# Kernel optimization log

Measured on AMD Instinct MI355X. Metric: run time of the kernel, lower is better.

## Reference

```python
import jax, jax.numpy as jnp
import numpy as np

B, L, P = 2, 1024, 1024
HID = 2048
NH, NKV, D = 32, 8, 64
T = P + L
N_REPEAT = NH // NKV
SCALE = D ** -0.5
NEG_INF = -1e9


def _rotate_half(x):
    x1, x2 = jnp.split(x, 2, axis=-1)
    return jnp.concatenate([-x2, x1], axis=-1)


def _apply_rope(q, k, cos, sin):
    # cos/sin: [L, D] -> broadcast to [1, 1, L, D]
    cos = cos[None, None, :, :]
    sin = sin[None, None, :, :]
    q = q * cos + _rotate_half(q) * sin
    k = k * cos + _rotate_half(k) * sin
    return q, k


def setup_inputs() -> dict:
    key = jax.random.key(0)
    ks = jax.random.split(key, 10)
    s = 0.02
    x = jax.random.normal(ks[0], (B, L, HID), jnp.float32)
    Wq = jax.random.normal(ks[1], (HID, NH * D), jnp.float32) * s
    bq = jnp.zeros((NH * D,), jnp.float32)
    Wk = jax.random.normal(ks[2], (HID, NKV * D), jnp.float32) * s
    bk = jnp.zeros((NKV * D,), jnp.float32)
    Wv = jax.random.normal(ks[3], (HID, NKV * D), jnp.float32) * s
    bv = jnp.zeros((NKV * D,), jnp.float32)
    Wo = jax.random.normal(ks[4], (NH * D, HID), jnp.float32) * s
    past_k = jax.random.normal(ks[5], (B, NKV, P, D), jnp.float32)
    past_v = jax.random.normal(ks[6], (B, NKV, P, D), jnp.float32)
    # RoPE tables for the L new positions (offsets P..P+L-1)
    pos = jnp.arange(P, P + L, dtype=jnp.float32)
    inv_freq = 1.0 / (10000.0 ** (jnp.arange(0, D, 2, dtype=jnp.float32) / D))
    freqs = pos[:, None] * inv_freq[None, :]            # [L, D/2]
    emb = jnp.concatenate([freqs, freqs], axis=-1)       # [L, D]
    cos = jnp.cos(emb)
    sin = jnp.sin(emb)
    # causal additive mask over total kv length T (past always visible)
    i = jnp.arange(L)[:, None]
    j = jnp.arange(T)[None, :]
    m = jnp.where(j <= i + P, 0.0, NEG_INF).astype(jnp.float32)  # [L, T]
    attention_mask = jnp.broadcast_to(m[None, None], (B, 1, L, T))
    return {
        "x": x, "attention_mask": attention_mask, "cos": cos, "sin": sin,
        "past_k": past_k, "past_v": past_v,
        "Wq": Wq, "bq": bq, "Wk": Wk, "bk": bk, "Wv": Wv, "bv": bv, "Wo": Wo,
    }


def reference(x, attention_mask, cos, sin, past_k, past_v, Wq, bq, Wk, bk, Wv, bv, Wo):
    # QKV projections
    q = (x @ Wq + bq).reshape(B, L, NH, D).transpose(0, 2, 1, 3)    # [B,NH,L,D]
    k = (x @ Wk + bk).reshape(B, L, NKV, D).transpose(0, 2, 1, 3)   # [B,NKV,L,D]
    v = (x @ Wv + bv).reshape(B, L, NKV, D).transpose(0, 2, 1, 3)
    q, k = _apply_rope(q, k, cos, sin)
    # KV-cache append
    k = jnp.concatenate([past_k, k], axis=2)  # [B,NKV,T,D]
    v = jnp.concatenate([past_v, v], axis=2)
    # repeat_kv for GQA
    if N_REPEAT > 1:
        k = jnp.repeat(k, N_REPEAT, axis=1)   # [B,NH,T,D]
        v = jnp.repeat(v, N_REPEAT, axis=1)
    w = jnp.einsum("bhld,bhtd->bhlt", q, k) * SCALE
    w = w + attention_mask
    w = jax.nn.softmax(w, axis=-1)
    out = jnp.einsum("bhlt,bhtd->bhld", w, v)
    out = out.transpose(0, 2, 1, 3).reshape(B, L, NH * D)
    return out @ Wo
```

## Files before the change

kernel.cpp:

```cpp
#include <hip/hip_runtime.h>
#include <stdint.h>

#define Bc   2
#define Lc   1024
#define Pc   1024
#define Tc   2048
#define HIDc 2048
#define NHc  32
#define NKVc 8
#define Dc   64

typedef __bf16 bf16x8 __attribute__((ext_vector_type(8)));
typedef float f32x4 __attribute__((ext_vector_type(4)));
typedef float f32x16 __attribute__((ext_vector_type(16)));

__device__ inline unsigned short f2bf(float f) {
  union { float f; uint32_t u; } v; v.f = f;
  uint32_t u = v.u;
  uint32_t r = (u + 0x7fffu + ((u >> 16) & 1u)) >> 16;
  return (unsigned short)r;
}
__device__ inline float bf2f(unsigned short h) {
  union { uint32_t u; float f; } v; v.u = ((uint32_t)h) << 16;
  return v.f;
}
__device__ inline float exp2_fast(float x) {
#if defined(__has_builtin)
#if __has_builtin(__builtin_amdgcn_exp2f)
  return __builtin_amdgcn_exp2f(x);
#else
  return exp2f(x);
#endif
#else
  return exp2f(x);
#endif
}
__device__ inline unsigned int cvtpk_bf16(float a, float b) {
  unsigned int r;
  asm("v_cvt_pk_bf16_f32 %0, %1, %2" : "=v"(r) : "v"(a), "v"(b));
  return r;
}
__device__ inline void plane32_swap(unsigned int& a, unsigned int& b) {
  asm("v_permlane32_swap_b32 %0, %1" : "+v"(a), "+v"(b));
}

typedef const __attribute__((address_space(1))) unsigned int* gas1_t;
typedef __attribute__((address_space(3))) unsigned int* las3_t;
__device__ inline void gload_lds16(const void* g, void* l) {
  __builtin_amdgcn_global_load_lds((gas1_t)g, (las3_t)l, 16, 0, 0);
}

__global__ void cast_x_kernel(const float* __restrict__ x, unsigned short* __restrict__ xb) {
  int i = (blockIdx.x * 256 + threadIdx.x) * 4;
  float4 v = *(const float4*)(x + i);
  ushort4 o;
  o.x = f2bf(v.x); o.y = f2bf(v.y); o.z = f2bf(v.z); o.w = f2bf(v.w);
  *(ushort4*)(xb + i) = o;
}

__global__ void transpose_all_kernel(const float* __restrict__ Wq, const float* __restrict__ Wk,
                                     const float* __restrict__ Wv, const float* __restrict__ Wo,
                                     unsigned short* __restrict__ WqkvT,
                                     unsigned short* __restrict__ WoT) {
  __shared__ float s[32][33];
  int bx = blockIdx.x, k0 = blockIdx.y * 32;
  const float* W;
  unsigned short* dst;
  int N, n0, drow;
  if (bx < 64)       { W = Wq; dst = WqkvT; N = 2048; n0 = bx * 32;        drow = n0; }
  else if (bx < 80)  { W = Wk; dst = WqkvT; N = 512;  n0 = (bx - 64) * 32; drow = 2048 + n0; }
  else if (bx < 96)  { W = Wv; dst = WqkvT; N = 512;  n0 = (bx - 80) * 32; drow = 2560 + n0; }
  else               { W = Wo; dst = WoT;   N = 2048; n0 = (bx - 96) * 32; drow = n0; }
  int tx = threadIdx.x, ty = threadIdx.y;
#pragma unroll
  for (int j = 0; j < 4; ++j)
    s[ty + j * 8][tx] = W[(size_t)(k0 + ty + j * 8) * N + n0 + tx];
  __syncthreads();
#pragma unroll
  for (int j = 0; j < 4; ++j)
    dst[(size_t)(drow + ty + j * 8) * 2048 + k0 + tx] = f2bf(s[tx][ty + j * 8]);
}

template <int TM, bool OUT_F32>
__global__ __launch_bounds__(256, 2) void gemm_kernel(
    const unsigned short* __restrict__ A, const unsigned short* __restrict__ BT,
    const float* __restrict__ bq, const float* __restrict__ bk, const float* __restrict__ bv,
    void* __restrict__ Cout, int N) {
  const int K = 2048;
  const int MI = TM / 32;
  __shared__ unsigned short sA[2][TM * 32];
  __shared__ unsigned short sB[2][128 * 32];
  const int m0 = blockIdx.y * TM, n0 = blockIdx.x * 128;
  const int tid = threadIdx.x;
  const int lane = tid & 63, w = tid >> 6;
  const int l15 = lane & 15, quad = lane >> 4;
  const int wm = (w & 1) * (TM / 2), wn = (w >> 1) * 64;

  f32x4 acc[MI][4];
#pragma unroll
  for (int i = 0; i < MI; ++i)
#pragma unroll
    for (int j = 0; j < 4; ++j) {
      f32x4 z = {0.f, 0.f, 0.f, 0.f};
      acc[i][j] = z;
    }

  const unsigned short* ga = A + (size_t)(m0 + (tid >> 2)) * K + (tid & 3) * 8;
  const unsigned short* gb = BT + (size_t)(n0 + (tid >> 2)) * K + (tid & 3) * 8;

  auto issue = [&](int tile, int buf) {
    int kb = tile * 32;
#pragma unroll
    for (int i = 0; i < TM / 64; ++i)
      gload_lds16(ga + (size_t)(i * 64) * K + kb, &sA[buf][i * 64 * 32 + tid * 8]);
    gload_lds16(gb + kb, &sB[buf][tid * 8]);
    gload_lds16(gb + (size_t)64 * K + kb, &sB[buf][64 * 32 + tid * 8]);
  };

  issue(0, 0);
  for (int t = 0; t < 64; ++t) {
    int tn = (t + 1 < 64) ? t + 1 : 63;
    issue(tn, (t + 1) & 1);
    if (TM == 128)
      asm volatile("s_waitcnt vmcnt(4)" ::: "memory");
    else
      asm volatile("s_waitcnt vmcnt(3)" ::: "memory");
    __builtin_amdgcn_s_barrier();
    const unsigned short* bA = sA[t & 1];
    const unsigned short* bB = sB[t & 1];
    bf16x8 af[MI], bfr[4];
#pragma unroll
    for (int i = 0; i < MI; ++i)
      af[i] = *(const bf16x8*)(bA + (wm + i * 16 + l15) * 32 + quad * 8);
#pragma unroll
    for (int i = 0; i < 4; ++i)
      bfr[i] = *(const bf16x8*)(bB + (wn + i * 16 + l15) * 32 + quad * 8);
#pragma unroll
    for (int mi = 0; mi < MI; ++mi)
#pragma unroll
      for (int ni = 0; ni < 4; ++ni)
        acc[mi][ni] = __builtin_amdgcn_mfma_f32_16x16x32_bf16(af[mi], bfr[ni], acc[mi][ni], 0, 0, 0);
    asm volatile("s_waitcnt lgkmcnt(0)" ::: "memory");
    __builtin_amdgcn_s_barrier();
  }

#pragma unroll
  for (int mi = 0; mi < MI; ++mi)
#pragma unroll
    for (int ni = 0; ni < 4; ++ni) {
      int col = n0 + wn + ni * 16 + l15;
      float bvv = 0.f;
      if (bq) bvv = (col < 2048) ? bq[col] : (col < 2560 ? bk[col - 2048] : bv[col - 2560]);
#pragma unroll
      for (int r = 0; r < 4; ++r) {
        int row = m0 + wm + mi * 16 + quad * 4 + r;
        float v = acc[mi][ni][r] + bvv;
        if (OUT_F32)
          ((float*)Cout)[(size_t)row * N + col] = v;
        else
          ((unsigned short*)Cout)[(size_t)row * N + col] = f2bf(v);
      }
    }
}

__global__ void build_kv_kernel(const unsigned short* __restrict__ qkv,
                                const float* __restrict__ past_k,
                                const float* __restrict__ past_v,
                                const float* __restrict__ cosb, const float* __restrict__ sinb,
                                unsigned short* __restrict__ Kc,
                                unsigned short* __restrict__ Vc) {
  __shared__ unsigned short s[32][72];
  int tid = threadIdx.x;
  if (blockIdx.x < 4096) {
    int idx = blockIdx.x * 256 + tid;
    int d = idx & 31;
    int t = (idx >> 5) & 2047;
    int bh = idx >> 16;
    size_t obase = ((size_t)bh * 2048 + t) * 64 + d;
    if (t < 1024) {
      size_t pb = ((size_t)bh * 1024 + t) * 64 + d;
      Kc[obase] = f2bf(past_k[pb]);
      Kc[obase + 32] = f2bf(past_k[pb + 32]);
    } else {
      int l = t - 1024;
      int b = bh >> 3, hk = bh & 7;
      size_t qb = ((size_t)(b * 1024 + l)) * 3072 + 2048 + hk * 64 + d;
      float k0 = bf2f(qkv[qb]), k1 = bf2f(qkv[qb + 32]);
      float c = cosb[l * 64 + d], sn = sinb[l * 64 + d];
      Kc[obase] = f2bf(k0 * c - k1 * sn);
      Kc[obase + 32] = f2bf(k1 * c + k0 * sn);
    }
  } else {
    int bx = blockIdx.x - 4096;
    int t0 = (bx & 63) * 32;
    int bh = bx >> 6;
#pragma unroll
    for (int i = 0; i < 8; ++i) {
      int e = tid + 256 * i;
      int tl = e >> 6, d = e & 63;
      int t = t0 + tl;
      unsigned short val;
      if (t < 1024) {
        val = f2bf(past_v[((size_t)bh * 1024 + t) * 64 + d]);
      } else {
        int b = bh >> 3, hk = bh & 7;
        int l = t - 1024;
        val = qkv[(size_t)(b * 1024 + l) * 3072 + 2560 + hk * 64 + d];
      }
      s[tl][d] = val;
    }
    __syncthreads();
#pragma unroll
    for (int i = 0; i < 8; ++i) {
      int e = tid + 256 * i;
      int d = e >> 5, tl = e & 31;
      Vc[((size_t)bh * 64 + d) * 2048 + t0 + tl] = s[tl][d];
    }
  }
}

__global__ __launch_bounds__(256, 2) void attn_kernel(
    const unsigned short* __restrict__ qkv,
    const unsigned short* __restrict__ Kc,
    const unsigned short* __restrict__ Vc,
    const float* __restrict__ cosb, const float* __restrict__ sinb,
    unsigned short* __restrict__ O) {
  __shared__ __align__(16) unsigned short sK[2][4096];
  __shared__ __align__(16) unsigned short sV[2][4096];

  int flat = blockIdx.x;
  int pair = (flat & 7) * 2 + ((flat >> 3) & 1);
  int b = pair >> 3, hk = pair & 7;
  int qt = flat >> 4;
  int q0 = qt * 32;

  const int tid = threadIdx.x;
  const int lane = tid & 63, w = tid >> 6;
  const int l31 = lane & 31, hh = lane >> 5;
  const int h = hk * 4 + w;

  union U8 { bf16x8 v; unsigned short u[8]; };
  union PB { unsigned int w4[4]; bf16x8 v; };

  const unsigned short* Kb = Kc + ((size_t)b * 8 + hk) * (2048 * 64);
  const unsigned short* Vb = Vc + ((size_t)b * 8 + hk) * (64 * 2048);

  const int sr = tid >> 3;
  const int sc = (tid & 7) * 8;
  const int ksw = sc >> 4;
  const int law = sr + ((sc >> 3) & 1) * 32;

  uint4 kreg0, kreg1, vreg0, vreg1;
  auto issueLoads = [&](int t0) {
    kreg0 = *(const uint4*)(Kb + (size_t)(t0 + sr) * 64 + sc);
    kreg1 = *(const uint4*)(Kb + (size_t)(t0 + sr + 32) * 64 + sc);
    vreg0 = *(const uint4*)(Vb + (size_t)sr * 2048 + t0 + sc);
    vreg1 = *(const uint4*)(Vb + (size_t)(sr + 32) * 2048 + t0 + sc);
  };
  auto writeStage = [&](int buf) {
    *(uint4*)(&sK[buf][(ksw * 64 + law) * 8]) = kreg0;
    *(uint4*)(&sK[buf][((4 + ksw) * 64 + law) * 8]) = kreg1;
    *(uint4*)(&sV[buf][(ksw * 64 + law) * 8]) = vreg0;
    *(uint4*)(&sV[buf][((4 + ksw) * 64 + law) * 8]) = vreg1;
  };

  issueLoads(0);

  const float SC = 0.125f * 1.44269504f;
  bf16x8 qB[4];
  {
    int row = q0 + l31;
    const unsigned short* qrow = qkv + (size_t)(b * 1024 + row) * 3072 + h * 64;
    U8 raw[4];
#pragma unroll
    for (int ks = 0; ks < 4; ++ks)
      raw[ks].v = *(const bf16x8*)(qrow + ks * 16 + hh * 8);
#pragma unroll
    for (int ks = 0; ks < 2; ++ks) {
      int dbase = ks * 16 + hh * 8;
      float4 ca = *(const float4*)(cosb + row * 64 + dbase);
      float4 cb = *(const float4*)(cosb + row * 64 + dbase + 4);
      float4 sa = *(const float4*)(sinb + row * 64 + dbase);
      float4 sb = *(const float4*)(sinb + row * 64 + dbase + 4);
      float c[8] = {ca.x, ca.y, ca.z, ca.w, cb.x, cb.y, cb.z, cb.w};
      float sn[8] = {sa.x, sa.y, sa.z, sa.w, sb.x, sb.y, sb.z, sb.w};
      U8 flo, fhi;
#pragma unroll
      for (int j = 0; j < 8; ++j) {
        float ql = bf2f(raw[ks].u[j]), qh = bf2f(raw[ks + 2].u[j]);
        float cc = c[j] * SC, ss = sn[j] * SC;
        flo.u[j] = f2bf(ql * cc - qh * ss);
        fhi.u[j] = f2bf(qh * cc + ql * ss);
      }
      qB[ks] = flo.v;
      qB[ks + 2] = fhi.v;
    }
  }

  f32x16 oaccT[2];
  {
    f32x16 z;
#pragma unroll
    for (int i = 0; i < 16; ++i) z[i] = 0.f;
    oaccT[0] = z; oaccT[1] = z;
  }
  float lsum = 0.f;

  const int ntile = (q0 + 32 + 1024 + 63) >> 6;

  writeStage(0);
  __syncthreads();

  for (int kt = 0; kt < ntile; ++kt) {
    int t0n = (kt + 1) * 64;
    if (t0n > 1984) t0n = 1984;
    issueLoads(t0n);

    const int t0 = kt * 64;
    const int buf = kt & 1;
    const unsigned short* bK = sK[buf];
    const unsigned short* bV = sV[buf];

    f32x16 sacc[2];
    {
      f32x16 z;
#pragma unroll
      for (int i = 0; i < 16; ++i) z[i] = 0.f;
      sacc[0] = z; sacc[1] = z;
    }
#pragma unroll
    for (int mf = 0; mf < 2; ++mf)
#pragma unroll
      for (int ks = 0; ks < 4; ++ks) {
        bf16x8 kf = *(const bf16x8*)(bK + ((mf * 4 + ks) * 64 + lane) * 8);
        sacc[mf] = __builtin_amdgcn_mfma_f32_32x32x16_bf16(kf, qB[ks], sacc[mf], 0, 0, 0);
      }

    unsigned int pk[2][8];
    const bool diag = (t0 + 63 > q0 + Pc);
    if (!diag) {
#pragma unroll
      for (int mf = 0; mf < 2; ++mf)
#pragma unroll
        for (int p = 0; p < 8; ++p) {
          float e0 = exp2_fast(sacc[mf][2 * p]);
          float e1 = exp2_fast(sacc[mf][2 * p + 1]);
          lsum += e0 + e1;
          pk[mf][p] = cvtpk_bf16(e0, e1);
        }
    } else {
      int rg = q0 + l31 + Pc;
#pragma unroll
      for (int mf = 0; mf < 2; ++mf)
#pragma unroll
        for (int p = 0; p < 8; ++p) {
          int r0 = 2 * p;
          int tg = t0 + mf * 32 + (r0 & 3) + 8 * (r0 >> 2) + 4 * hh;
          float e0 = (tg <= rg) ? exp2_fast(sacc[mf][r0]) : 0.f;
          float e1 = (tg + 1 <= rg) ? exp2_fast(sacc[mf][r0 + 1]) : 0.f;
          lsum += e0 + e1;
          pk[mf][p] = cvtpk_bf16(e0, e1);
        }
    }

    PB pb[4];
#pragma unroll
    for (int ks = 0; ks < 4; ++ks) {
      int mf = ks >> 1, o = (ks & 1) * 4;
      unsigned int a0 = pk[mf][o + 0], b0 = pk[mf][o + 2];
      unsigned int a1 = pk[mf][o + 1], b1 = pk[mf][o + 3];
      plane32_swap(a0, b0);
      plane32_swap(a1, b1);
      pb[ks].w4[0] = a0; pb[ks].w4[1] = a1; pb[ks].w4[2] = b0; pb[ks].w4[3] = b1;
    }

#pragma unroll
    for (int md = 0; md < 2; ++md)
#pragma unroll
      for (int ks = 0; ks < 4; ++ks) {
        bf16x8 vA = *(const bf16x8*)(bV + ((md * 4 + ks) * 64 + lane) * 8);
        oaccT[md] = __builtin_amdgcn_mfma_f32_32x32x16_bf16(vA, pb[ks].v, oaccT[md], 0, 0, 0);
      }

    writeStage(buf ^ 1);
    __syncthreads();
  }

  lsum += __shfl_xor(lsum, 32);
  float inv = 1.f / lsum;
  int row = b * 1024 + q0 + l31;
#pragma unroll
  for (int md = 0; md < 2; ++md)
#pragma unroll
    for (int g = 0; g < 4; ++g) {
      int dbase = md * 32 + 8 * g + 4 * hh;
      ushort4 ov;
      ov.x = f2bf(oaccT[md][4 * g + 0] * inv);
      ov.y = f2bf(oaccT[md][4 * g + 1] * inv);
      ov.z = f2bf(oaccT[md][4 * g + 2] * inv);
      ov.w = f2bf(oaccT[md][4 * g + 3] * inv);
      *(ushort4*)(O + (size_t)row * 2048 + h * 64 + dbase) = ov;
    }
}

extern "C" void kernel_launch(void* const* d_in, const int* in_sizes, int n_in,
                              void* d_out, int out_size, void* d_ws, size_t ws_size,
                              hipStream_t stream) {
  const float* x      = (const float*)d_in[0];
  const float* cosb   = (const float*)d_in[2];
  const float* sinb   = (const float*)d_in[3];
  const float* past_k = (const float*)d_in[4];
  const float* past_v = (const float*)d_in[5];
  const float* Wq     = (const float*)d_in[6];
  const float* bq     = (const float*)d_in[7];
  const float* Wk     = (const float*)d_in[8];
  const float* bk     = (const float*)d_in[9];
  const float* Wv     = (const float*)d_in[10];
  const float* bv     = (const float*)d_in[11];
  const float* Wo     = (const float*)d_in[12];
  float* out = (float*)d_out;

  char* ws = (char*)d_ws;
  unsigned short* xb    = (unsigned short*)(ws + ((size_t)0 << 20));
  unsigned short* WqkvT = (unsigned short*)(ws + ((size_t)8 << 20));
  unsigned short* WoT   = (unsigned short*)(ws + ((size_t)20 << 20));
  unsigned short* qkvb  = (unsigned short*)(ws + ((size_t)28 << 20));
  unsigned short* Kc    = (unsigned short*)(ws + ((size_t)40 << 20));
  unsigned short* Vc    = (unsigned short*)(ws + ((size_t)44 << 20));
  unsigned short* attno = (unsigned short*)(ws + ((size_t)48 << 20));

  cast_x_kernel<<<4096, 256, 0, stream>>>(x, xb);
  transpose_all_kernel<<<dim3(160, 64), dim3(32, 8), 0, stream>>>(Wq, Wk, Wv, Wo, WqkvT, WoT);

  gemm_kernel<64, false><<<dim3(24, 32), 256, 0, stream>>>(xb, WqkvT, bq, bk, bv, qkvb, 3072);

  build_kv_kernel<<<5120, 256, 0, stream>>>(qkvb, past_k, past_v, cosb, sinb, Kc, Vc);

  attn_kernel<<<512, 256, 0, stream>>>(qkvb, Kc, Vc, cosb, sinb, attno);

  gemm_kernel<64, true><<<dim3(16, 32), 256, 0, stream>>>(attno, WoT, nullptr, nullptr, nullptr, out, 2048);
}
```

Measured before the change: 278.4 us.

## Split KV range across waves and pre-swizzle K/V into MFMA fragment layout

build_kv now writes K and V tiles already arranged in MFMA fragment order, so attention waves can load operands straight from global memory without LDS staging or barriers. The attention kernel moves from one head per wave to one head per block, with the four waves splitting the KV tiles between them (split-K). Partial outputs and row sums are combined through shared memory at the end. The grid grows from 512 to 2048 blocks with launch bounds raised to 4 blocks per CU, which adds parallelism. In exchange, K/V reuse across the four GQA heads now relies on L2 rather than shared memory, and the final reduction adds LDS traffic.

Result: faster. 261.9 us (-5.9%).

```diff
diff --git a/kernel.cpp b/kernel.cpp
--- a/kernel.cpp
+++ b/kernel.cpp
@@ -169,102 +169,105 @@
                                 const float* __restrict__ cosb, const float* __restrict__ sinb,
                                 unsigned short* __restrict__ Kc,
                                 unsigned short* __restrict__ Vc) {
-  __shared__ unsigned short s[32][72];
-  int tid = threadIdx.x;
-  if (blockIdx.x < 4096) {
-    int idx = blockIdx.x * 256 + tid;
-    int d = idx & 31;
-    int t = (idx >> 5) & 2047;
-    int bh = idx >> 16;
-    size_t obase = ((size_t)bh * 2048 + t) * 64 + d;
-    if (t < 1024) {
-      size_t pb = ((size_t)bh * 1024 + t) * 64 + d;
-      Kc[obase] = f2bf(past_k[pb]);
-      Kc[obase + 32] = f2bf(past_k[pb + 32]);
-    } else {
-      int l = t - 1024;
-      int b = bh >> 3, hk = bh & 7;
-      size_t qb = ((size_t)(b * 1024 + l)) * 3072 + 2048 + hk * 64 + d;
-      float k0 = bf2f(qkv[qb]), k1 = bf2f(qkv[qb + 32]);
-      float c = cosb[l * 64 + d], sn = sinb[l * 64 + d];
-      Kc[obase] = f2bf(k0 * c - k1 * sn);
-      Kc[obase + 32] = f2bf(k1 * c + k0 * sn);
-    }
+  __shared__ __align__(16) unsigned short sK[64 * 72];
+  __shared__ __align__(16) unsigned short sVT[64 * 72];
+  union U8 { bf16x8 v; unsigned short u[8]; };
+
+  const int bid = blockIdx.x;
+  const int bh = bid >> 5, tt = bid & 31;
+  const int b = bh >> 3, hk = bh & 7;
+  const int tid = threadIdx.x;
+  const int tl = tid >> 2;
+  const int c16 = (tid & 3) * 16;
+
+  const int t = tt * 64 + tl;
+
+  U8 ko0, ko1;
+  if (tt < 16) {
+    const float* src = past_k + (((size_t)bh * 1024 + t) * 64 + c16);
+#pragma unroll
+    for (int i = 0; i < 8; ++i) ko0.u[i] = f2bf(src[i]);
+#pragma unroll
+    for (int i = 0; i < 8; ++i) ko1.u[i] = f2bf(src[8 + i]);
   } else {
-    int bx = blockIdx.x - 4096;
-    int t0 = (bx & 63) * 32;
-    int bh = bx >> 6;
-#pragma unroll
-    for (int i = 0; i < 8; ++i) {
-      int e = tid + 256 * i;
-      int tl = e >> 6, d = e & 63;
-      int t = t0 + tl;
-      unsigned short val;
-      if (t < 1024) {
-        val = f2bf(past_v[((size_t)bh * 1024 + t) * 64 + d]);
-      } else {
-        int b = bh >> 3, hk = bh & 7;
-        int l = t - 1024;
-        val = qkv[(size_t)(b * 1024 + l) * 3072 + 2560 + hk * 64 + d];
-      }
-      s[tl][d] = val;
-    }
-    __syncthreads();
-#pragma unroll
-    for (int i = 0; i < 8; ++i) {
-      int e = tid + 256 * i;
-      int d = e >> 5, tl = e & 31;
-      Vc[((size_t)bh * 64 + d) * 2048 + t0 + tl] = s[tl][d];
-    }
-  }
-}
-
-__global__ __launch_bounds__(256, 2) void attn_kernel(
+    const int l = t - 1024;
+    const unsigned short* krow = qkv + ((size_t)(b * 1024 + l)) * 3072 + 2048 + hk * 64;
+    const int po = (c16 < 32) ? 32 : -32;
+    const float sgn = (c16 < 32) ? -1.f : 1.f;
+    U8 own0, own1, par0, par1;
+    own0.v = *(const bf16x8*)(krow + c16);
+    own1.v = *(const bf16x8*)(krow + c16 + 8);
+    par0.v = *(const bf16x8*)(krow + c16 + po);
+    par1.v = *(const bf16x8*)(krow + c16 + po + 8);
+    const float* cb = cosb + l * 64 + c16;
+    const float* sb = sinb + l * 64 + c16;
+#pragma unroll
+    for (int i = 0; i < 8; ++i)
+      ko0.u[i] = f2bf(bf2f(own0.u[i]) * cb[i] + sgn * bf2f(par0.u[i]) * sb[i]);
+#pragma unroll
+    for (int i = 0; i < 8; ++i)
+      ko1.u[i] = f2bf(bf2f(own1.u[i]) * cb[8 + i] + sgn * bf2f(par1.u[i]) * sb[8 + i]);
+  }
+  *(bf16x8*)&sK[tl * 72 + c16] = ko0.v;
+  *(bf16x8*)&sK[tl * 72 + c16 + 8] = ko1.v;
+
+  if (tt < 16) {
+    const float* src = past_v + (((size_t)bh * 1024 + t) * 64 + c16);
+#pragma unroll
+    for (int i = 0; i < 16; ++i) sVT[(c16 + i) * 72 + tl] = f2bf(src[i]);
+  } else {
+    const unsigned short* vrow = qkv + ((size_t)(b * 1024 + (t - 1024))) * 3072 + 2560 + hk * 64 + c16;
+    U8 v0, v1;
+    v0.v = *(const bf16x8*)(vrow);
+    v1.v = *(const bf16x8*)(vrow + 8);
+#pragma unroll
+    for (int i = 0; i < 8; ++i) sVT[(c16 + i) * 72 + tl] = v0.u[i];
+#pragma unroll
+    for (int i = 0; i < 8; ++i) sVT[(c16 + 8 + i) * 72 + tl] = v1.u[i];
+  }
+
+  __syncthreads();
+
+  unsigned short* KD = Kc + (size_t)bh * 131072 + (size_t)tt * 4096;
+  unsigned short* VD = Vc + (size_t)bh * 131072 + (size_t)tt * 4096;
+#pragma unroll
+  for (int half = 0; half < 2; ++half) {
+    int c = tid + half * 256;
+    int f = c >> 6, l = c & 63;
+    int col = (f & 3) * 16 + (l >> 5) * 8;
+    int row = (f >> 2) * 32 + (l & 31);
+    *(bf16x8*)(KD + f * 512 + l * 8) = *(const bf16x8*)&sK[row * 72 + col];
+    *(bf16x8*)(VD + f * 512 + l * 8) = *(const bf16x8*)&sVT[row * 72 + col];
+  }
+}
+
+__global__ __launch_bounds__(256, 4) void attn_kernel(
     const unsigned short* __restrict__ qkv,
     const unsigned short* __restrict__ Kc,
     const unsigned short* __restrict__ Vc,
     const float* __restrict__ cosb, const float* __restrict__ sinb,
     unsigned short* __restrict__ O) {
-  __shared__ __align__(16) unsigned short sK[2][4096];
-  __shared__ __align__(16) unsigned short sV[2][4096];
-
-  int flat = blockIdx.x;
-  int pair = (flat & 7) * 2 + ((flat >> 3) & 1);
-  int b = pair >> 3, hk = pair & 7;
-  int qt = flat >> 4;
-  int q0 = qt * 32;
+  __shared__ float comb[4][32][68];
+  __shared__ float lsmem[4][32];
+
+  const int flat = blockIdx.x;
+  const int hk = flat & 7;
+  const int b = (flat >> 3) & 1;
+  const int h2 = (flat >> 4) & 3;
+  const int qt = flat >> 6;
+  const int h = hk * 4 + h2;
+  const int q0 = qt * 32;
+  const int bh = b * 8 + hk;
 
   const int tid = threadIdx.x;
   const int lane = tid & 63, w = tid >> 6;
   const int l31 = lane & 31, hh = lane >> 5;
-  const int h = hk * 4 + w;
 
   union U8 { bf16x8 v; unsigned short u[8]; };
   union PB { unsigned int w4[4]; bf16x8 v; };
 
-  const unsigned short* Kb = Kc + ((size_t)b * 8 + hk) * (2048 * 64);
-  const unsigned short* Vb = Vc + ((size_t)b * 8 + hk) * (64 * 2048);
-
-  const int sr = tid >> 3;
-  const int sc = (tid & 7) * 8;
-  const int ksw = sc >> 4;
-  const int law = sr + ((sc >> 3) & 1) * 32;
-
-  uint4 kreg0, kreg1, vreg0, vreg1;
-  auto issueLoads = [&](int t0) {
-    kreg0 = *(const uint4*)(Kb + (size_t)(t0 + sr) * 64 + sc);
-    kreg1 = *(const uint4*)(Kb + (size_t)(t0 + sr + 32) * 64 + sc);
-    vreg0 = *(const uint4*)(Vb + (size_t)sr * 2048 + t0 + sc);
-    vreg1 = *(const uint4*)(Vb + (size_t)(sr + 32) * 2048 + t0 + sc);
-  };
-  auto writeStage = [&](int buf) {
-    *(uint4*)(&sK[buf][(ksw * 64 + law) * 8]) = kreg0;
-    *(uint4*)(&sK[buf][((4 + ksw) * 64 + law) * 8]) = kreg1;
-    *(uint4*)(&sV[buf][(ksw * 64 + law) * 8]) = vreg0;
-    *(uint4*)(&sV[buf][((4 + ksw) * 64 + law) * 8]) = vreg1;
-  };
-
-  issueLoads(0);
+  const unsigned short* KT = Kc + (size_t)bh * 131072;
+  const unsigned short* VT = Vc + (size_t)bh * 131072;
 
   const float SC = 0.125f * 1.44269504f;
   bf16x8 qB[4];
@@ -306,20 +309,14 @@
   }
   float lsum = 0.f;
 
-  const int ntile = (q0 + 32 + 1024 + 63) >> 6;
-
-  writeStage(0);
-  __syncthreads();
-
-  for (int kt = 0; kt < ntile; ++kt) {
-    int t0n = (kt + 1) * 64;
-    if (t0n > 1984) t0n = 1984;
-    issueLoads(t0n);
-
-    const int t0 = kt * 64;
-    const int buf = kt & 1;
-    const unsigned short* bK = sK[buf];
-    const unsigned short* bV = sV[buf];
+  const int ntile = (q0 + 1119) >> 6;
+
+  for (int kt = w; kt < ntile; kt += 4) {
+    const unsigned short* kb = KT + (size_t)kt * 4096 + lane * 8;
+
+    bf16x8 kf[8];
+#pragma unroll
+    for (int f = 0; f < 8; ++f) kf[f] = *(const bf16x8*)(kb + f * 512);
 
     f32x16 sacc[2];
     {
@@ -329,13 +326,13 @@
       sacc[0] = z; sacc[1] = z;
     }
 #pragma unroll
-    for (int mf = 0; mf < 2; ++mf)
-#pragma unroll
-      for (int ks = 0; ks < 4; ++ks) {
-        bf16x8 kf = *(const bf16x8*)(bK + ((mf * 4 + ks) * 64 + lane) * 8);
-        sacc[mf] = __builtin_amdgcn_mfma_f32_32x32x16_bf16(kf, qB[ks], sacc[mf], 0, 0, 0);
-      }
-
+    for (int ks = 0; ks < 4; ++ks)
+      sacc[0] = __builtin_amdgcn_mfma_f32_32x32x16_bf16(kf[ks], qB[ks], sacc[0], 0, 0, 0);
+#pragma unroll
+    for (int ks = 0; ks < 4; ++ks)
+      sacc[1] = __builtin_amdgcn_mfma_f32_32x32x16_bf16(kf[4 + ks], qB[ks], sacc[1], 0, 0, 0);
+
+    const int t0 = kt * 64;
     unsigned int pk[2][8];
     const bool diag = (t0 + 63 > q0 + Pc);
     if (!diag) {
@@ -363,6 +360,11 @@
         }
     }
 
+    const unsigned short* vb = VT + (size_t)kt * 4096 + lane * 8;
+    bf16x8 vf[8];
+#pragma unroll
+    for (int f = 0; f < 8; ++f) vf[f] = *(const bf16x8*)(vb + f * 512);
+
     PB pb[4];
 #pragma unroll
     for (int ks = 0; ks < 4; ++ks) {
@@ -377,30 +379,41 @@
 #pragma unroll
     for (int md = 0; md < 2; ++md)
 #pragma unroll
-      for (int ks = 0; ks < 4; ++ks) {
-        bf16x8 vA = *(const bf16x8*)(bV + ((md * 4 + ks) * 64 + lane) * 8);
-        oaccT[md] = __builtin_amdgcn_mfma_f32_32x32x16_bf16(vA, pb[ks].v, oaccT[md], 0, 0, 0);
-      }
-
-    writeStage(buf ^ 1);
-    __syncthreads();
+      for (int ks = 0; ks < 4; ++ks)
+        oaccT[md] = __builtin_amdgcn_mfma_f32_32x32x16_bf16(vf[md * 4 + ks], pb[ks].v, oaccT[md], 0, 0, 0);
   }
 
   lsum += __shfl_xor(lsum, 32);
-  float inv = 1.f / lsum;
-  int row = b * 1024 + q0 + l31;
+  if (hh == 0) lsmem[w][l31] = lsum;
 #pragma unroll
   for (int md = 0; md < 2; ++md)
 #pragma unroll
     for (int g = 0; g < 4; ++g) {
-      int dbase = md * 32 + 8 * g + 4 * hh;
-      ushort4 ov;
-      ov.x = f2bf(oaccT[md][4 * g + 0] * inv);
-      ov.y = f2bf(oaccT[md][4 * g + 1] * inv);
-      ov.z = f2bf(oaccT[md][4 * g + 2] * inv);
-      ov.w = f2bf(oaccT[md][4 * g + 3] * inv);
-      *(ushort4*)(O + (size_t)row * 2048 + h * 64 + dbase) = ov;
-    }
+      float4 fv = {oaccT[md][4 * g + 0], oaccT[md][4 * g + 1],
+                   oaccT[md][4 * g + 2], oaccT[md][4 * g + 3]};
+      *(float4*)&comb[w][l31][md * 32 + 8 * g + 4 * hh] = fv;
+    }
+  __syncthreads();
+
+  const int q = tid >> 3, c8 = (tid & 7) * 8;
+  float a8[8];
+#pragma unroll
+  for (int i = 0; i < 8; ++i) a8[i] = 0.f;
+#pragma unroll
+  for (int wv = 0; wv < 4; ++wv) {
+    float4 p0 = *(const float4*)&comb[wv][q][c8];
+    float4 p1 = *(const float4*)&comb[wv][q][c8 + 4];
+    a8[0] += p0.x; a8[1] += p0.y; a8[2] += p0.z; a8[3] += p0.w;
+    a8[4] += p1.x; a8[5] += p1.y; a8[6] += p1.z; a8[7] += p1.w;
+  }
+  float linv = 1.f / (lsmem[0][q] + lsmem[1][q] + lsmem[2][q] + lsmem[3][q]);
+  uint4 ov;
+  ov.x = cvtpk_bf16(a8[0] * linv, a8[1] * linv);
+  ov.y = cvtpk_bf16(a8[2] * linv, a8[3] * linv);
+  ov.z = cvtpk_bf16(a8[4] * linv, a8[5] * linv);
+  ov.w = cvtpk_bf16(a8[6] * linv, a8[7] * linv);
+  int row = b * 1024 + q0 + q;
+  *(uint4*)(O + (size_t)row * 2048 + h * 64 + c8) = ov;
 }
 
 extern "C" void kernel_launch(void* const* d_in, const int* in_sizes, int n_in,
@@ -434,9 +447,9 @@
 
   gemm_kernel<64, false><<<dim3(24, 32), 256, 0, stream>>>(xb, WqkvT, bq, bk, bv, qkvb, 3072);
 
-  build_kv_kernel<<<5120, 256, 0, stream>>>(qkvb, past_k, past_v, cosb, sinb, Kc, Vc);
-
-  attn_kernel<<<512, 256, 0, stream>>>(qkvb, Kc, Vc, cosb, sinb, attno);
+  build_kv_kernel<<<512, 256, 0, stream>>>(qkvb, past_k, past_v, cosb, sinb, Kc, Vc);
+
+  attn_kernel<<<2048, 256, 0, stream>>>(qkvb, Kc, Vc, cosb, sinb, attno);
 
   gemm_kernel<64, true><<<dim3(16, 32), 256, 0, stream>>>(attno, WoT, nullptr, nullptr, nullptr, out, 2048);
 }
```
